# Kernel optimization log

Measured on AMD Instinct MI355X. Metric: run time of the kernel, lower is better.

Reference implementation:

```python
import jax, jax.numpy as jnp
import numpy as np

BINS = 64

def _histc_rows(flat, bins):
    # flat: [N, L]; per-row torch.histc semantics with min=max=0 (use data min/max)
    lo = flat.min(axis=1, keepdims=True)
    hi = flat.max(axis=1, keepdims=True)
    same = hi == lo
    lo = jnp.where(same, lo - 1.0, lo)
    hi = jnp.where(same, hi + 1.0, hi)
    # bin index; value == hi maps to bins -> clipped into last bin (torch includes max)
    idx = jnp.floor((flat - lo) / (hi - lo) * bins).astype(jnp.int32)
    idx = jnp.clip(idx, 0, bins - 1)
    n = flat.shape[0]
    flat_idx = idx + (jnp.arange(n, dtype=jnp.int32)[:, None] * bins)
    hist = jnp.zeros((n * bins,), dtype=flat.dtype).at[flat_idx.ravel()].add(1.0)
    return hist.reshape(n, bins)

def reference(x, conv_w, conv_b, head_w, head_b):
    # Conv2d(1 -> C, k=3, valid), NCHW
    y = jax.lax.conv_general_dilated(
        x, conv_w, window_strides=(1, 1), padding='VALID',
        dimension_numbers=('NCHW', 'OIHW', 'NCHW'))
    y = y + conv_b[None, :, None, None]
    y = jax.nn.relu(y)
    b, c, h, w = y.shape
    hist = _histc_rows(y.reshape(b * c, h * w), BINS)  # [B*C, bins]
    feat = hist.reshape(b, c * BINS)
    return feat @ head_w.T + head_b

def setup_inputs() -> dict:
    key = jax.random.key(0)
    k1, k2, k3, k4, k5 = jax.random.split(key, 5)
    C, K, F = 64, 3, 1000
    return {
        'x': jax.random.normal(k1, (64, 1, 256, 256), dtype=jnp.float32),
        'conv_w': jax.random.normal(k2, (C, 1, K, K), dtype=jnp.float32) * 0.1,
        'conv_b': jax.random.normal(k3, (C,), dtype=jnp.float32) * 0.1,
        'head_w': jax.random.normal(k4, (F, C * BINS), dtype=jnp.float32) * 0.02,
        'head_b': jax.random.normal(k5, (F,), dtype=jnp.float32) * 0.02,
    }
```

## Files before the change

### kernel.cpp

```cpp
#include <hip/hip_runtime.h>


typedef short bf16x8 __attribute__((ext_vector_type(8)));
typedef float f32x16 __attribute__((ext_vector_type(16)));

#define TPITCH 35
#define F_OUT_ 1000
#define KDIM_ 4096

__device__ __forceinline__ unsigned f2bf(float f) {
    unsigned u = __float_as_uint(f);
    return (u + 0x7FFFu + ((u >> 16) & 1u)) >> 16;
}
__device__ __forceinline__ float bf2f(unsigned h) { return __uint_as_float(h << 16); }

__device__ __forceinline__ unsigned cvt_u32_sat(float f) {
    unsigned r;
    asm volatile("v_cvt_u32_f32 %0, %1" : "=v"(r) : "v"(f));
    return r;
}

union FragU { uint4 u; bf16x8 v; };

__global__ __launch_bounds__(512, 6) void conv_minmax_kernel(
    const float* __restrict__ x, const float* __restrict__ cw,
    const float* __restrict__ cb, float* __restrict__ featQ,
    float* __restrict__ mnbuf, float* __restrict__ mxbuf)
{
    __shared__ unsigned t32[256 * TPITCH];
    __shared__ float red[1024];

    const int tid = threadIdx.x;
    const int lane = tid & 63;
    const int w = __builtin_amdgcn_readfirstlane(tid >> 6);
    const int b = blockIdx.x;
    const int seg = blockIdx.y;
    const int mrow = lane & 31;
    const int kg = lane >> 5;
    const int r0 = seg * 32;
    const int vlim = min(32, 254 - r0);

    featQ[(seg * 64 + b) * 512 + tid] = 0.f;

    FragU bwh[2], bwl[2];
#pragma unroll
    for (int g = 0; g < 2; ++g) {
        int och = g * 32 + mrow;
        unsigned hh[8], ll[8];
#pragma unroll
        for (int j = 0; j < 8; ++j) {
            int k = kg * 8 + j, dr = k >> 2, dc = k & 3;
            float wv = (kg == 1 && j == 7) ? cb[och]
                     : ((dr < 3 && dc < 3) ? cw[och * 9 + dr * 3 + dc] : 0.f);
            unsigned h = f2bf(wv);
            hh[j] = h;
            ll[j] = f2bf(wv - bf2f(h));
        }
        bwh[g].u = make_uint4(hh[0] | (hh[1] << 16), hh[2] | (hh[3] << 16),
                              hh[4] | (hh[5] << 16), hh[6] | (hh[7] << 16));
        bwl[g].u = make_uint4(ll[0] | (ll[1] << 16), ll[2] | (ll[3] << 16),
                              ll[4] | (ll[5] << 16), ll[6] | (ll[7] << 16));
    }
    f32x16 zc;
#pragma unroll
    for (int r = 0; r < 16; ++r) zc[r] = 0.f;

    const float* xb = x + (size_t)b * 65536;
    for (int i = tid; i < TPITCH * 256; i += 512) {
        int lrow = i >> 8, col = i & 255;
        int grow = r0 + lrow;
        float v = (grow < 256) ? xb[grow * 256 + col] : 0.f;
        unsigned h = f2bf(v);
        unsigned l = f2bf(v - bf2f(h));
        t32[col * TPITCH + lrow] = (l << 16) | h;
    }
    __syncthreads();

    float mnA = 3.4e38f, mxA = -3.4e38f;
    float mnB = 3.4e38f, mxB = -3.4e38f;
    const int cbase = w * 32;
    const int cend = min(cbase + 32, 254);
    const unsigned* tb = t32 + mrow + 2 * kg;
    unsigned a0 = tb[cbase * TPITCH],       r1a = tb[cbase * TPITCH + 1];
    unsigned a1 = tb[(cbase + 1) * TPITCH], r1b = tb[(cbase + 1) * TPITCH + 1];
    unsigned a2 = tb[(cbase + 2) * TPITCH], r1c = tb[(cbase + 2) * TPITCH + 1];
#pragma unroll 2
    for (int c = cbase; c < cend; ++c) {
        int cp = min(c + 3, 255);
        unsigned a3  = tb[cp * TPITCH];
        unsigned r1d = tb[cp * TPITCH + 1];
        FragU ah, al;
        ah.u = make_uint4(__builtin_amdgcn_perm(a1, a0, 0x05040100u), a2,
                          __builtin_amdgcn_perm(r1b, r1a, 0x05040100u),
                          (r1c & 0xFFFFu) | 0x3F800000u);
        al.u = make_uint4(__builtin_amdgcn_perm(a1, a0, 0x07060302u), a2 >> 16,
                          __builtin_amdgcn_perm(r1b, r1a, 0x07060302u), r1c >> 16);
        a0 = a1; a1 = a2; a2 = a3; r1a = r1b; r1b = r1c; r1c = r1d;
        f32x16 accA = __builtin_amdgcn_mfma_f32_32x32x16_bf16(ah.v, bwh[0].v, zc, 0, 0, 0);
        f32x16 accB = __builtin_amdgcn_mfma_f32_32x32x16_bf16(ah.v, bwh[1].v, zc, 0, 0, 0);
        accA = __builtin_amdgcn_mfma_f32_32x32x16_bf16(al.v, bwh[0].v, accA, 0, 0, 0);
        accB = __builtin_amdgcn_mfma_f32_32x32x16_bf16(al.v, bwh[1].v, accB, 0, 0, 0);
        accA = __builtin_amdgcn_mfma_f32_32x32x16_bf16(ah.v, bwl[0].v, accA, 0, 0, 0);
        accB = __builtin_amdgcn_mfma_f32_32x32x16_bf16(ah.v, bwl[1].v, accB, 0, 0, 0);
        if (vlim >= 32) {
#pragma unroll
            for (int r = 0; r < 16; r += 2) {
                mnA = fminf(fminf(mnA, accA[r]), accA[r + 1]);
                mxA = fmaxf(fmaxf(mxA, accA[r]), accA[r + 1]);
                mnB = fminf(fminf(mnB, accB[r]), accB[r + 1]);
                mxB = fmaxf(fmaxf(mxB, accB[r]), accB[r + 1]);
            }
        } else {
#pragma unroll
            for (int r = 0; r < 16; ++r) {
                int crow = (r & 3) + 8 * (r >> 2) + 4 * kg;
                float vA = (crow < vlim) ? accA[r] : accA[0];
                float vB = (crow < vlim) ? accB[r] : accB[0];
                mnA = fminf(mnA, vA); mxA = fmaxf(mxA, vA);
                mnB = fminf(mnB, vB); mxB = fmaxf(mxB, vB);
            }
        }
    }

    mnA = fminf(mnA, __shfl_xor(mnA, 32, 64));
    mxA = fmaxf(mxA, __shfl_xor(mxA, 32, 64));
    mnB = fminf(mnB, __shfl_xor(mnB, 32, 64));
    mxB = fmaxf(mxB, __shfl_xor(mxB, 32, 64));
    __syncthreads();
    if (lane < 32) {
        red[w * 64 + mrow] = mnA;        red[512 + w * 64 + mrow] = mxA;
        red[w * 64 + 32 + mrow] = mnB;   red[512 + w * 64 + 32 + mrow] = mxB;
    }
    __syncthreads();
    if (tid < 64) {
        float a = red[tid], c = red[512 + tid];
#pragma unroll
        for (int i = 1; i < 8; ++i) {
            a = fminf(a, red[i * 64 + tid]);
            c = fmaxf(c, red[512 + i * 64 + tid]);
        }
        mnbuf[((b * 64 + tid) << 3) | seg] = a;
        mxbuf[((b * 64 + tid) << 3) | seg] = c;
    }
}

__global__ __launch_bounds__(512, 6) void conv_hist_kernel(
    const float* __restrict__ x, const float* __restrict__ cw,
    const float* __restrict__ cb, float* __restrict__ featQ,
    const float* __restrict__ mnbuf, const float* __restrict__ mxbuf)
{
    __shared__ unsigned t32[256 * TPITCH];
    __shared__ unsigned hist[65 * 32];

    const int tid = threadIdx.x;
    const int lane = tid & 63;
    const int w = __builtin_amdgcn_readfirstlane(tid >> 6);
    const int b = blockIdx.x;
    const int seg = blockIdx.y;
    const int gz = blockIdx.z;
    const int mrow = lane & 31;
    const int kg = lane >> 5;
    const int r0 = seg * 32;
    const int vlim = min(32, 254 - r0);
    const int och = gz * 32 + mrow;

    float rmn = 3.402823466e38f, rmx = -3.402823466e38f;
#pragma unroll
    for (int s = 0; s < 8; ++s) {
        rmn = fminf(rmn, mnbuf[((b * 64 + och) << 3) | s]);
        rmx = fmaxf(rmx, mxbuf[((b * 64 + och) << 3) | s]);
    }
    float lo = fmaxf(rmn, 0.f);
    float hi = fmaxf(rmx, 0.f);
    if (hi == lo) { lo -= 1.f; hi += 1.f; }
    const float sc = 63.984f / (hi - lo);
    const float nls = -lo * sc;
    for (int i = tid; i < 65 * 32; i += 512) hist[i] = 0u;

    FragU bwh, bwl;
    {
        unsigned hh[8], ll[8];
#pragma unroll
        for (int j = 0; j < 8; ++j) {
            int k = kg * 8 + j, dr = k >> 2, dc = k & 3;
            float wv = (kg == 1 && j == 7) ? fmaf(cb[och], sc, nls)
                     : ((dr < 3 && dc < 3) ? cw[och * 9 + dr * 3 + dc] * sc : 0.f);
            unsigned h = f2bf(wv);
            hh[j] = h;
            ll[j] = f2bf(wv - bf2f(h));
        }
        bwh.u = make_uint4(hh[0] | (hh[1] << 16), hh[2] | (hh[3] << 16),
                           hh[4] | (hh[5] << 16), hh[6] | (hh[7] << 16));
        bwl.u = make_uint4(ll[0] | (ll[1] << 16), ll[2] | (ll[3] << 16),
                           ll[4] | (ll[5] << 16), ll[6] | (ll[7] << 16));
    }
    f32x16 zc;
#pragma unroll
    for (int r = 0; r < 16; ++r) zc[r] = 0.f;

    const float* xb = x + (size_t)b * 65536;
    for (int i = tid; i < TPITCH * 256; i += 512) {
        int lrow = i >> 8, col = i & 255;
        int grow = r0 + lrow;
        float v = (grow < 256) ? xb[grow * 256 + col] : 0.f;
        unsigned h = f2bf(v);
        unsigned l = f2bf(v - bf2f(h));
        t32[col * TPITCH + lrow] = (l << 16) | h;
    }
    __syncthreads();

    const int cbase = w * 32;
    const int cend = min(cbase + 32, 254);
    unsigned* hrow = hist + mrow;
    const unsigned* tb = t32 + mrow + 2 * kg;
    unsigned a0 = tb[cbase * TPITCH],       r1a = tb[cbase * TPITCH + 1];
    unsigned a1 = tb[(cbase + 1) * TPITCH], r1b = tb[(cbase + 1) * TPITCH + 1];
    unsigned a2 = tb[(cbase + 2) * TPITCH], r1c = tb[(cbase + 2) * TPITCH + 1];
#pragma unroll 2
    for (int c = cbase; c < cend; ++c) {
        int cp = min(c + 3, 255);
        unsigned a3  = tb[cp * TPITCH];
        unsigned r1d = tb[cp * TPITCH + 1];
        FragU ah, al;
        ah.u = make_uint4(__builtin_amdgcn_perm(a1, a0, 0x05040100u), a2,
                          __builtin_amdgcn_perm(r1b, r1a, 0x05040100u),
                          (r1c & 0xFFFFu) | 0x3F800000u);
        al.u = make_uint4(__builtin_amdgcn_perm(a1, a0, 0x07060302u), a2 >> 16,
                          __builtin_amdgcn_perm(r1b, r1a, 0x07060302u), r1c >> 16);
        a0 = a1; a1 = a2; a2 = a3; r1a = r1b; r1b = r1c; r1c = r1d;
        f32x16 acc = __builtin_amdgcn_mfma_f32_32x32x16_bf16(ah.v, bwh.v, zc, 0, 0, 0);
        acc = __builtin_amdgcn_mfma_f32_32x32x16_bf16(al.v, bwh.v, acc, 0, 0, 0);
        acc = __builtin_amdgcn_mfma_f32_32x32x16_bf16(ah.v, bwl.v, acc, 0, 0, 0);
        if (vlim >= 32) {
#pragma unroll
            for (int r = 0; r < 16; ++r) {
                unsigned bin = cvt_u32_sat(acc[r]);
                atomicAdd(&hrow[bin << 5], 1u);
            }
        } else {
#pragma unroll
            for (int r = 0; r < 16; ++r) {
                int crow = (r & 3) + 8 * (r >> 2) + 4 * kg;
                unsigned bin = cvt_u32_sat(acc[r]);
                if (crow >= vlim) bin = 64u;
                atomicAdd(&hrow[bin << 5], 1u);
            }
        }
    }
    __syncthreads();

    for (int i = tid; i < 2048; i += 512) {
        int o = i >> 6, bin = i & 63;
        float cnt = (float)hist[(bin << 5) + o];
        int k = ((gz * 32 + o) << 6) | bin;
        atomicAdd(&featQ[((k >> 2) << 8) | (b << 2) | (k & 3)], cnt);
    }
}

__global__ __launch_bounds__(256) void head_kernel(
    const float* __restrict__ featQ, const float* __restrict__ hw,
    float* __restrict__ part)
{
    __shared__ float red[4][8][64];
    const int tid = threadIdx.x;
    const int m = tid & 63;
    const int kh = __builtin_amdgcn_readfirstlane(tid >> 6);
    const int n0 = blockIdx.x * 8;
    const int q = blockIdx.y;
    const int kqbase = q * 64 + kh * 16;
    const float* fb = featQ + kqbase * 256 + (m << 2);
    const float* wp[8];
#pragma unroll
    for (int c = 0; c < 8; ++c)
        wp[c] = hw + (size_t)(n0 + c) * KDIM_ + (kqbase << 2);

    float a[8] = {0.f, 0.f, 0.f, 0.f, 0.f, 0.f, 0.f, 0.f};
#pragma unroll 2
    for (int kq = 0; kq < 16; ++kq) {
        float4 f = *(const float4*)(fb + (kq << 8));
#pragma unroll
        for (int c = 0; c < 8; ++c) {
            float4 u = *(const float4*)(wp[c] + (kq << 2));
            a[c] += f.x * u.x + f.y * u.y + f.z * u.z + f.w * u.w;
        }
    }
#pragma unroll
    for (int c = 0; c < 8; ++c) red[kh][c][m] = a[c];
    __syncthreads();
    for (int s = tid; s < 512; s += 256) {
        int c = s >> 6, mm = s & 63;
        float v = red[0][c][mm] + red[1][c][mm] + red[2][c][mm] + red[3][c][mm];
        part[(size_t)q * 64000 + (n0 + c) * 64 + mm] = v;
    }
}

__global__ __launch_bounds__(256) void head_reduce_kernel(
    const float* __restrict__ part, const float* __restrict__ hb,
    float* __restrict__ out)
{
    int idx = blockIdx.x * 256 + threadIdx.x;
    int n = idx >> 6, m = idx & 63;
    float v = hb[n];
#pragma unroll
    for (int q = 0; q < 16; ++q) v += part[q * 64000 + idx];
    out[(size_t)m * F_OUT_ + n] = v;
}

extern "C" void kernel_launch(void* const* d_in, const int* in_sizes, int n_in,
                              void* d_out, int out_size, void* d_ws, size_t ws_size,
                              hipStream_t stream) {
    const float* x      = (const float*)d_in[0];
    const float* conv_w = (const float*)d_in[1];
    const float* conv_b = (const float*)d_in[2];
    const float* head_w = (const float*)d_in[3];
    const float* head_b = (const float*)d_in[4];
    float* out   = (float*)d_out;
    float* featQ = (float*)d_ws;
    float* mnbuf = featQ + 262144;
    float* mxbuf = mnbuf + 32768;
    float* part  = mxbuf + 32768;

    dim3 g1(64, 8);
    dim3 g2(64, 8, 2);
    conv_minmax_kernel<<<g1, 512, 0, stream>>>(x, conv_w, conv_b, featQ, mnbuf, mxbuf);
    conv_hist_kernel<<<g2, 512, 0, stream>>>(x, conv_w, conv_b, featQ, mnbuf, mxbuf);
    head_kernel<<<dim3(125, 16), 256, 0, stream>>>(featQ, head_w, part);
    head_reduce_kernel<<<250, 256, 0, stream>>>(part, head_b, out);
}
```

Baseline: 178.3 us.

## Split minmax kernel by channel group, pack 16-bit histogram counters, shrink LDS pitch

```diff
diff --git a/kernel.cpp b/kernel.cpp
--- a/kernel.cpp
+++ b/kernel.cpp
@@ -4,7 +4,7 @@
 typedef short bf16x8 __attribute__((ext_vector_type(8)));
 typedef float f32x16 __attribute__((ext_vector_type(16)));
 
-#define TPITCH 35
+#define TPITCH 34
 #define F_OUT_ 1000
 #define KDIM_ 4096
 
@@ -22,135 +22,13 @@
 
 union FragU { uint4 u; bf16x8 v; };
 
-__global__ __launch_bounds__(512, 6) void conv_minmax_kernel(
+__global__ __launch_bounds__(512, 8) void conv_minmax_kernel(
     const float* __restrict__ x, const float* __restrict__ cw,
     const float* __restrict__ cb, float* __restrict__ featQ,
     float* __restrict__ mnbuf, float* __restrict__ mxbuf)
 {
     __shared__ unsigned t32[256 * TPITCH];
-    __shared__ float red[1024];
-
-    const int tid = threadIdx.x;
-    const int lane = tid & 63;
-    const int w = __builtin_amdgcn_readfirstlane(tid >> 6);
-    const int b = blockIdx.x;
-    const int seg = blockIdx.y;
-    const int mrow = lane & 31;
-    const int kg = lane >> 5;
-    const int r0 = seg * 32;
-    const int vlim = min(32, 254 - r0);
-
-    featQ[(seg * 64 + b) * 512 + tid] = 0.f;
-
-    FragU bwh[2], bwl[2];
-#pragma unroll
-    for (int g = 0; g < 2; ++g) {
-        int och = g * 32 + mrow;
-        unsigned hh[8], ll[8];
-#pragma unroll
-        for (int j = 0; j < 8; ++j) {
-            int k = kg * 8 + j, dr = k >> 2, dc = k & 3;
-            float wv = (kg == 1 && j == 7) ? cb[och]
-                     : ((dr < 3 && dc < 3) ? cw[och * 9 + dr * 3 + dc] : 0.f);
-            unsigned h = f2bf(wv);
-            hh[j] = h;
-            ll[j] = f2bf(wv - bf2f(h));
-        }
-        bwh[g].u = make_uint4(hh[0] | (hh[1] << 16), hh[2] | (hh[3] << 16),
-                              hh[4] | (hh[5] << 16), hh[6] | (hh[7] << 16));
-        bwl[g].u = make_uint4(ll[0] | (ll[1] << 16), ll[2] | (ll[3] << 16),
-                              ll[4] | (ll[5] << 16), ll[6] | (ll[7] << 16));
-    }
-    f32x16 zc;
-#pragma unroll
-    for (int r = 0; r < 16; ++r) zc[r] = 0.f;
-
-    const float* xb = x + (size_t)b * 65536;
-    for (int i = tid; i < TPITCH * 256; i += 512) {
-        int lrow = i >> 8, col = i & 255;
-        int grow = r0 + lrow;
-        float v = (grow < 256) ? xb[grow * 256 + col] : 0.f;
-        unsigned h = f2bf(v);
-        unsigned l = f2bf(v - bf2f(h));
-        t32[col * TPITCH + lrow] = (l << 16) | h;
-    }
-    __syncthreads();
-
-    float mnA = 3.4e38f, mxA = -3.4e38f;
-    float mnB = 3.4e38f, mxB = -3.4e38f;
-    const int cbase = w * 32;
-    const int cend = min(cbase + 32, 254);
-    const unsigned* tb = t32 + mrow + 2 * kg;
-    unsigned a0 = tb[cbase * TPITCH],       r1a = tb[cbase * TPITCH + 1];
-    unsigned a1 = tb[(cbase + 1) * TPITCH], r1b = tb[(cbase + 1) * TPITCH + 1];
-    unsigned a2 = tb[(cbase + 2) * TPITCH], r1c = tb[(cbase + 2) * TPITCH + 1];
-#pragma unroll 2
-    for (int c = cbase; c < cend; ++c) {
-        int cp = min(c + 3, 255);
-        unsigned a3  = tb[cp * TPITCH];
-        unsigned r1d = tb[cp * TPITCH + 1];
-        FragU ah, al;
-        ah.u = make_uint4(__builtin_amdgcn_perm(a1, a0, 0x05040100u), a2,
-                          __builtin_amdgcn_perm(r1b, r1a, 0x05040100u),
-                          (r1c & 0xFFFFu) | 0x3F800000u);
-        al.u = make_uint4(__builtin_amdgcn_perm(a1, a0, 0x07060302u), a2 >> 16,
-                          __builtin_amdgcn_perm(r1b, r1a, 0x07060302u), r1c >> 16);
-        a0 = a1; a1 = a2; a2 = a3; r1a = r1b; r1b = r1c; r1c = r1d;
-        f32x16 accA = __builtin_amdgcn_mfma_f32_32x32x16_bf16(ah.v, bwh[0].v, zc, 0, 0, 0);
-        f32x16 accB = __builtin_amdgcn_mfma_f32_32x32x16_bf16(ah.v, bwh[1].v, zc, 0, 0, 0);
-        accA = __builtin_amdgcn_mfma_f32_32x32x16_bf16(al.v, bwh[0].v, accA, 0, 0, 0);
-        accB = __builtin_amdgcn_mfma_f32_32x32x16_bf16(al.v, bwh[1].v, accB, 0, 0, 0);
-        accA = __builtin_amdgcn_mfma_f32_32x32x16_bf16(ah.v, bwl[0].v, accA, 0, 0, 0);
-        accB = __builtin_amdgcn_mfma_f32_32x32x16_bf16(ah.v, bwl[1].v, accB, 0, 0, 0);
-        if (vlim >= 32) {
-#pragma unroll
-            for (int r = 0; r < 16; r += 2) {
-                mnA = fminf(fminf(mnA, accA[r]), accA[r + 1]);
-                mxA = fmaxf(fmaxf(mxA, accA[r]), accA[r + 1]);
-                mnB = fminf(fminf(mnB, accB[r]), accB[r + 1]);
-                mxB = fmaxf(fmaxf(mxB, accB[r]), accB[r + 1]);
-            }
-        } else {
-#pragma unroll
-            for (int r = 0; r < 16; ++r) {
-                int crow = (r & 3) + 8 * (r >> 2) + 4 * kg;
-                float vA = (crow < vlim) ? accA[r] : accA[0];
-                float vB = (crow < vlim) ? accB[r] : accB[0];
-                mnA = fminf(mnA, vA); mxA = fmaxf(mxA, vA);
-                mnB = fminf(mnB, vB); mxB = fmaxf(mxB, vB);
-            }
-        }
-    }
-
-    mnA = fminf(mnA, __shfl_xor(mnA, 32, 64));
-    mxA = fmaxf(mxA, __shfl_xor(mxA, 32, 64));
-    mnB = fminf(mnB, __shfl_xor(mnB, 32, 64));
-    mxB = fmaxf(mxB, __shfl_xor(mxB, 32, 64));
-    __syncthreads();
-    if (lane < 32) {
-        red[w * 64 + mrow] = mnA;        red[512 + w * 64 + mrow] = mxA;
-        red[w * 64 + 32 + mrow] = mnB;   red[512 + w * 64 + 32 + mrow] = mxB;
-    }
-    __syncthreads();
-    if (tid < 64) {
-        float a = red[tid], c = red[512 + tid];
-#pragma unroll
-        for (int i = 1; i < 8; ++i) {
-            a = fminf(a, red[i * 64 + tid]);
-            c = fmaxf(c, red[512 + i * 64 + tid]);
-        }
-        mnbuf[((b * 64 + tid) << 3) | seg] = a;
-        mxbuf[((b * 64 + tid) << 3) | seg] = c;
-    }
-}
-
-__global__ __launch_bounds__(512, 6) void conv_hist_kernel(
-    const float* __restrict__ x, const float* __restrict__ cw,
-    const float* __restrict__ cb, float* __restrict__ featQ,
-    const float* __restrict__ mnbuf, const float* __restrict__ mxbuf)
-{
-    __shared__ unsigned t32[256 * TPITCH];
-    __shared__ unsigned hist[65 * 32];
+    __shared__ float red[512];
 
     const int tid = threadIdx.x;
     const int lane = tid & 63;
@@ -164,18 +42,7 @@
     const int vlim = min(32, 254 - r0);
     const int och = gz * 32 + mrow;
 
-    float rmn = 3.402823466e38f, rmx = -3.402823466e38f;
-#pragma unroll
-    for (int s = 0; s < 8; ++s) {
-        rmn = fminf(rmn, mnbuf[((b * 64 + och) << 3) | s]);
-        rmx = fmaxf(rmx, mxbuf[((b * 64 + och) << 3) | s]);
-    }
-    float lo = fmaxf(rmn, 0.f);
-    float hi = fmaxf(rmx, 0.f);
-    if (hi == lo) { lo -= 1.f; hi += 1.f; }
-    const float sc = 63.984f / (hi - lo);
-    const float nls = -lo * sc;
-    for (int i = tid; i < 65 * 32; i += 512) hist[i] = 0u;
+    if (gz == 0) featQ[(seg * 64 + b) * 512 + tid] = 0.f;
 
     FragU bwh, bwl;
     {
@@ -183,8 +50,8 @@
 #pragma unroll
         for (int j = 0; j < 8; ++j) {
             int k = kg * 8 + j, dr = k >> 2, dc = k & 3;
-            float wv = (kg == 1 && j == 7) ? fmaf(cb[och], sc, nls)
-                     : ((dr < 3 && dc < 3) ? cw[och * 9 + dr * 3 + dc] * sc : 0.f);
+            float wv = (kg == 1 && j == 7) ? cb[och]
+                     : ((dr < 3 && dc < 3) ? cw[och * 9 + dr * 3 + dc] : 0.f);
             unsigned h = f2bf(wv);
             hh[j] = h;
             ll[j] = f2bf(wv - bf2f(h));
@@ -209,9 +76,9 @@
     }
     __syncthreads();
 
+    float mn = 3.4e38f, mx = -3.4e38f;
     const int cbase = w * 32;
     const int cend = min(cbase + 32, 254);
-    unsigned* hrow = hist + mrow;
     const unsigned* tb = t32 + mrow + 2 * kg;
     unsigned a0 = tb[cbase * TPITCH],       r1a = tb[cbase * TPITCH + 1];
     unsigned a1 = tb[(cbase + 1) * TPITCH], r1b = tb[(cbase + 1) * TPITCH + 1];
@@ -233,9 +100,132 @@
         acc = __builtin_amdgcn_mfma_f32_32x32x16_bf16(ah.v, bwl.v, acc, 0, 0, 0);
         if (vlim >= 32) {
 #pragma unroll
+            for (int r = 0; r < 16; r += 2) {
+                mn = fminf(fminf(mn, acc[r]), acc[r + 1]);
+                mx = fmaxf(fmaxf(mx, acc[r]), acc[r + 1]);
+            }
+        } else {
+#pragma unroll
+            for (int r = 0; r < 16; ++r) {
+                int crow = (r & 3) + 8 * (r >> 2) + 4 * kg;
+                float v = (crow < vlim) ? acc[r] : acc[0];
+                mn = fminf(mn, v); mx = fmaxf(mx, v);
+            }
+        }
+    }
+
+    mn = fminf(mn, __shfl_xor(mn, 32, 64));
+    mx = fmaxf(mx, __shfl_xor(mx, 32, 64));
+    __syncthreads();
+    if (lane < 32) {
+        red[w * 32 + mrow] = mn;
+        red[256 + w * 32 + mrow] = mx;
+    }
+    __syncthreads();
+    if (tid < 32) {
+        float a = red[tid], c = red[256 + tid];
+#pragma unroll
+        for (int i = 1; i < 8; ++i) {
+            a = fminf(a, red[i * 32 + tid]);
+            c = fmaxf(c, red[256 + i * 32 + tid]);
+        }
+        mnbuf[((b * 64 + gz * 32 + tid) << 3) | seg] = a;
+        mxbuf[((b * 64 + gz * 32 + tid) << 3) | seg] = c;
+    }
+}
+
+__global__ __launch_bounds__(512, 8) void conv_hist_kernel(
+    const float* __restrict__ x, const float* __restrict__ cw,
+    const float* __restrict__ cb, float* __restrict__ featQ,
+    const float* __restrict__ mnbuf, const float* __restrict__ mxbuf)
+{
+    __shared__ unsigned t32[256 * TPITCH];
+    __shared__ unsigned hist[65 * 16];
+    const int tid = threadIdx.x;
+    const int lane = tid & 63;
+    const int w = __builtin_amdgcn_readfirstlane(tid >> 6);
+    const int b = blockIdx.x;
+    const int seg = blockIdx.y;
+    const int gz = blockIdx.z;
+    const int mrow = lane & 31;
+    const int kg = lane >> 5;
+    const int r0 = seg * 32;
+    const int vlim = min(32, 254 - r0);
+    const int och = gz * 32 + mrow;
+
+    float rmn = 3.402823466e38f, rmx = -3.402823466e38f;
+#pragma unroll
+    for (int s = 0; s < 8; ++s) {
+        rmn = fminf(rmn, mnbuf[((b * 64 + och) << 3) | s]);
+        rmx = fmaxf(rmx, mxbuf[((b * 64 + och) << 3) | s]);
+    }
+    float lo = fmaxf(rmn, 0.f);
+    float hi = fmaxf(rmx, 0.f);
+    if (hi == lo) { lo -= 1.f; hi += 1.f; }
+    const float sc = 63.984f / (hi - lo);
+    const float nls = -lo * sc;
+    for (int i = tid; i < 65 * 16; i += 512) hist[i] = 0u;
+
+    FragU bwh, bwl;
+    {
+        unsigned hh[8], ll[8];
+#pragma unroll
+        for (int j = 0; j < 8; ++j) {
+            int k = kg * 8 + j, dr = k >> 2, dc = k & 3;
+            float wv = (kg == 1 && j == 7) ? fmaf(cb[och], sc, nls)
+                     : ((dr < 3 && dc < 3) ? cw[och * 9 + dr * 3 + dc] * sc : 0.f);
+            unsigned h = f2bf(wv);
+            hh[j] = h;
+            ll[j] = f2bf(wv - bf2f(h));
+        }
+        bwh.u = make_uint4(hh[0] | (hh[1] << 16), hh[2] | (hh[3] << 16),
+                           hh[4] | (hh[5] << 16), hh[6] | (hh[7] << 16));
+        bwl.u = make_uint4(ll[0] | (ll[1] << 16), ll[2] | (ll[3] << 16),
+                           ll[4] | (ll[5] << 16), ll[6] | (ll[7] << 16));
+    }
+    f32x16 zc;
+#pragma unroll
+    for (int r = 0; r < 16; ++r) zc[r] = 0.f;
+
+    const float* xb = x + (size_t)b * 65536;
+    for (int i = tid; i < TPITCH * 256; i += 512) {
+        int lrow = i >> 8, col = i & 255;
+        int grow = r0 + lrow;
+        float v = (grow < 256) ? xb[grow * 256 + col] : 0.f;
+        unsigned h = f2bf(v);
+        unsigned l = f2bf(v - bf2f(h));
+        t32[col * TPITCH + lrow] = (l << 16) | h;
+    }
+    __syncthreads();
+
+    const int cbase = w * 32;
+    const int cend = min(cbase + 32, 254);
+    const unsigned addv = (mrow < 16) ? 1u : 65536u;
+    unsigned* hrow = hist + (mrow & 15);
+    const unsigned* tb = t32 + mrow + 2 * kg;
+    unsigned a0 = tb[cbase * TPITCH],       r1a = tb[cbase * TPITCH + 1];
+    unsigned a1 = tb[(cbase + 1) * TPITCH], r1b = tb[(cbase + 1) * TPITCH + 1];
+    unsigned a2 = tb[(cbase + 2) * TPITCH], r1c = tb[(cbase + 2) * TPITCH + 1];
+#pragma unroll 2
+    for (int c = cbase; c < cend; ++c) {
+        int cp = min(c + 3, 255);
+        unsigned a3  = tb[cp * TPITCH];
+        unsigned r1d = tb[cp * TPITCH + 1];
+        FragU ah, al;
+        ah.u = make_uint4(__builtin_amdgcn_perm(a1, a0, 0x05040100u), a2,
+                          __builtin_amdgcn_perm(r1b, r1a, 0x05040100u),
+                          (r1c & 0xFFFFu) | 0x3F800000u);
+        al.u = make_uint4(__builtin_amdgcn_perm(a1, a0, 0x07060302u), a2 >> 16,
+                          __builtin_amdgcn_perm(r1b, r1a, 0x07060302u), r1c >> 16);
+        a0 = a1; a1 = a2; a2 = a3; r1a = r1b; r1b = r1c; r1c = r1d;
+        f32x16 acc = __builtin_amdgcn_mfma_f32_32x32x16_bf16(ah.v, bwh.v, zc, 0, 0, 0);
+        acc = __builtin_amdgcn_mfma_f32_32x32x16_bf16(al.v, bwh.v, acc, 0, 0, 0);
+        acc = __builtin_amdgcn_mfma_f32_32x32x16_bf16(ah.v, bwl.v, acc, 0, 0, 0);
+        if (vlim >= 32) {
+#pragma unroll
             for (int r = 0; r < 16; ++r) {
                 unsigned bin = cvt_u32_sat(acc[r]);
-                atomicAdd(&hrow[bin << 5], 1u);
+                atomicAdd(&hrow[bin << 4], addv);
             }
         } else {
 #pragma unroll
@@ -243,15 +233,16 @@
                 int crow = (r & 3) + 8 * (r >> 2) + 4 * kg;
                 unsigned bin = cvt_u32_sat(acc[r]);
                 if (crow >= vlim) bin = 64u;
-                atomicAdd(&hrow[bin << 5], 1u);
+                atomicAdd(&hrow[bin << 4], addv);
             }
         }
     }
     __syncthreads();
 
     for (int i = tid; i < 2048; i += 512) {
-        int o = i >> 6, bin = i & 63;
-        float cnt = (float)hist[(bin << 5) + o];
+        int bin = i >> 5, o = i & 31;
+        unsigned wv = hist[(bin << 4) + (o & 15)];
+        float cnt = (float)((o < 16) ? (wv & 0xFFFFu) : (wv >> 16));
         int k = ((gz * 32 + o) << 6) | bin;
         atomicAdd(&featQ[((k >> 2) << 8) | (b << 2) | (k & 3)], cnt);
     }
@@ -320,7 +311,7 @@
     float* mxbuf = mnbuf + 32768;
     float* part  = mxbuf + 32768;
 
-    dim3 g1(64, 8);
+    dim3 g1(64, 8, 2);
     dim3 g2(64, 8, 2);
     conv_minmax_kernel<<<g1, 512, 0, stream>>>(x, conv_w, conv_b, featQ, mnbuf, mxbuf);
     conv_hist_kernel<<<g2, 512, 0, stream>>>(x, conv_w, conv_b, featQ, mnbuf, mxbuf);
```

Result: slower. 219.3 us (+23.0%).
